# Optimization experiments

Hardware: AMD Instinct MI355X
Metric: run time of the kernel (lower is better)

## Reference

```python
import jax, jax.numpy as jnp
import numpy as np

EPS = 1e-5
P = 8  # patch size


def ln_chan(x, w, b):
    # LayerNorm over channel dim C of (B,C,H,W): per-pixel mean/var across channels
    mu = x.mean(axis=1, keepdims=True)
    var = x.var(axis=1, keepdims=True)
    return (x - mu) / jnp.sqrt(var + EPS) * w[None, :, None, None] + b[None, :, None, None]


def conv1x1(x, w):
    # w: (O, C) -> pointwise conv
    return jnp.einsum('bchw,oc->bohw', x, w)


def dwconv3(x, w):
    # depthwise 3x3, SAME padding; w: (C,1,3,3)
    return jax.lax.conv_general_dilated(
        x, w, window_strides=(1, 1), padding='SAME',
        dimension_numbers=('NCHW', 'OIHW', 'NCHW'),
        feature_group_count=x.shape[1])


def to_patches(t):
    b, c, h, w = t.shape
    return t.reshape(b, c, h // P, P, w // P, P).transpose(0, 1, 2, 4, 3, 5)


def from_patches(t, h, w):
    b, c = t.shape[:2]
    return t.transpose(0, 1, 2, 4, 3, 5).reshape(b, c, h, w)


def setup_inputs() -> dict:
    key = jax.random.key(0)
    ks = jax.random.split(key, 8)
    B, C, H, W = 4, 64, 256, 256
    s = 0.1  # weight scale to keep activations sane
    inp = {
        'x': jax.random.normal(ks[0], (B, C, H, W), jnp.float32),
        'evt': jax.random.normal(ks[1], (B, C, H, W), jnp.float32),
        'w_q': jax.random.normal(ks[2], (2 * C, C), jnp.float32) * s,
        'w_kv': jax.random.normal(ks[3], (4 * C, C), jnp.float32) * s,
        'w_qdw': jax.random.normal(ks[4], (2 * C, 1, 3, 3), jnp.float32) * s,
        'w_kvdw': jax.random.normal(ks[5], (4 * C, 1, 3, 3), jnp.float32) * s,
        'w_proj': jax.random.normal(ks[6], (C, 2 * C), jnp.float32) * s,
        'ln_img_w': jnp.ones((C,), jnp.float32),
        'ln_img_b': jnp.zeros((C,), jnp.float32),
        'ln_evt_w': jnp.ones((C,), jnp.float32),
        'ln_evt_b': jnp.zeros((C,), jnp.float32),
        'ln_out_w': jnp.ones((2 * C,), jnp.float32),
        'ln_out_b': jnp.zeros((2 * C,), jnp.float32),
    }
    return inp


def reference(x, evt, w_q, w_kv, w_qdw, w_kvdw, w_proj,
              ln_img_w, ln_img_b, ln_evt_w, ln_evt_b, ln_out_w, ln_out_b):
    x = ln_chan(x, ln_img_w, ln_img_b)
    evt = ln_chan(evt, ln_evt_w, ln_evt_b)
    q = dwconv3(conv1x1(x, w_q), w_qdw)          # (B, 2C, H, W)
    kv = dwconv3(conv1x1(evt, w_kv), w_kvdw)     # (B, 4C, H, W)
    k, v = jnp.split(kv, 2, axis=1)
    h, w = q.shape[-2:]
    q_fft = jnp.fft.rfft2(to_patches(q))         # (B,2C,h/8,w/8,8,5) complex
    k_fft = jnp.fft.rfft2(to_patches(k))
    out = jnp.fft.irfft2(q_fft * k_fft, s=(P, P))
    out = from_patches(out, h, w)                # (B, 2C, H, W)
    out = ln_chan(out, ln_out_w, ln_out_b)
    out = v * out
    return conv1x1(out, w_proj)                  # (B, C, H, W)
```

## Files before the change

### kernel.cpp

```cpp
#include <hip/hip_runtime.h>

typedef __attribute__((ext_vector_type(8))) short bf16x8;
typedef __attribute__((ext_vector_type(4))) float f32x4;
typedef __attribute__((ext_vector_type(2))) float f32x2;
typedef __attribute__((ext_vector_type(4))) unsigned int u32x4;
typedef __attribute__((ext_vector_type(2))) unsigned int u32x2;

__device__ __forceinline__ unsigned short f2bf(float f) {
    union { float f; unsigned int u; } v; v.f = f;
    return (unsigned short)((v.u + 0x7fffu + ((v.u >> 16) & 1u)) >> 16);
}
__device__ __forceinline__ float bflo(unsigned int u) {
    union { unsigned int u; float f; } v; v.u = u << 16; return v.f;
}
__device__ __forceinline__ float bfhi(unsigned int u) {
    union { unsigned int u; float f; } v; v.u = u & 0xffff0000u; return v.f;
}
__device__ __forceinline__ f32x2 bfpair(unsigned int u) {
    union { unsigned int u; float f; } lo, hi;
    lo.u = u << 16; hi.u = u & 0xffff0000u;
    return (f32x2){lo.f, hi.f};
}

__device__ __forceinline__ unsigned short costab(int m) {
    unsigned short mag = (m & 1) ? 0x3F35 : (((m & 3) == 0) ? 0x3F80 : 0);
    return mag | (((m >= 3) && (m <= 5)) ? 0x8000 : 0);
}
__device__ __forceinline__ unsigned short nsintab(int m) {
    unsigned short mag = (m & 1) ? 0x3F35 : (((m & 3) == 2) ? 0x3F80 : 0);
    return mag | (((m >= 1) && (m <= 3)) ? 0x8000 : 0);
}

__device__ __forceinline__ float wred_allsum(float x) {
    asm volatile(
        "s_nop 1\n\t"
        "v_add_f32_dpp %0, %0, %0 row_shr:1 bound_ctrl:0\n\t"
        "s_nop 1\n\t"
        "v_add_f32_dpp %0, %0, %0 row_shr:2 bound_ctrl:0\n\t"
        "s_nop 1\n\t"
        "v_add_f32_dpp %0, %0, %0 row_shr:4 bound_ctrl:0\n\t"
        "s_nop 1\n\t"
        "v_add_f32_dpp %0, %0, %0 row_shr:8 bound_ctrl:0\n\t"
        "s_nop 1\n\t"
        "v_add_f32_dpp %0, %0, %0 row_bcast:15 row_mask:0xa bound_ctrl:0\n\t"
        "s_nop 1\n\t"
        "v_add_f32_dpp %0, %0, %0 row_bcast:31 row_mask:0xc bound_ctrl:0\n\t"
        "s_nop 1"
        : "+v"(x));
    return __builtin_bit_cast(float, __builtin_amdgcn_readlane(__builtin_bit_cast(int, x), 63));
}

__global__ __launch_bounds__(256, 8)
void ln_kernel(const float* __restrict__ x, const float* __restrict__ evt,
               const float* __restrict__ lwx, const float* __restrict__ lbx,
               const float* __restrict__ lwe, const float* __restrict__ lbe,
               unsigned short* __restrict__ xo, unsigned short* __restrict__ eo)
{
    __shared__ float xt[64][68];
    __shared__ float ps[4][64], ps2[4][64];
    __shared__ float smu[64], sinv[64], slw[64], slb[64];

    const int tid = threadIdx.x;
    const int z = blockIdx.z, b = blockIdx.y;
    const int hw0 = blockIdx.x * 64;
    const float* src = z ? evt : x;
    const float* lw  = z ? lwe : lwx;
    const float* lb  = z ? lbe : lbx;
    unsigned short* dst = z ? eo : xo;

    if (tid < 64) { slw[tid] = lw[tid]; slb[tid] = lb[tid]; }

    const float* sp = src + (size_t)b * 64 * 65536 + hw0;
    #pragma unroll
    for (int it = 0; it < 4; ++it) {
        int i = tid + it * 256;
        int c = i >> 4, p4 = i & 15;
        f32x4 v = *(const f32x4*)&sp[(size_t)c * 65536 + p4 * 4];
        xt[p4 * 4 + 0][c] = v.x;
        xt[p4 * 4 + 1][c] = v.y;
        xt[p4 * 4 + 2][c] = v.z;
        xt[p4 * 4 + 3][c] = v.w;
    }
    __syncthreads();

    {
        int px = tid & 63, part = tid >> 6;
        float s = 0.f, s2 = 0.f;
        #pragma unroll
        for (int j = 0; j < 4; ++j) {
            f32x4 v = *(const f32x4*)&xt[px][part * 16 + j * 4];
            s  += v.x + v.y + v.z + v.w;
            s2 += v.x * v.x + v.y * v.y + v.z * v.z + v.w * v.w;
        }
        ps[part][px] = s; ps2[part][px] = s2;
    }
    __syncthreads();
    if (tid < 64) {
        float s  = ps[0][tid] + ps[1][tid] + ps[2][tid] + ps[3][tid];
        float s2 = ps2[0][tid] + ps2[1][tid] + ps2[2][tid] + ps2[3][tid];
        float mu = s * (1.f / 64.f);
        smu[tid] = mu;
        sinv[tid] = rsqrtf(s2 * (1.f / 64.f) - mu * mu + 1e-5f);
    }
    __syncthreads();

    unsigned short* dp = dst + ((size_t)b * 65536 + hw0) * 64;
    #pragma unroll
    for (int it = 0; it < 2; ++it) {
        int i = tid + it * 256;
        int px = i >> 3, oct = i & 7;
        float mu = smu[px], inv = sinv[px];
        f32x4 v0 = *(const f32x4*)&xt[px][oct * 8];
        f32x4 v1 = *(const f32x4*)&xt[px][oct * 8 + 4];
        u32x4 w;
        int c = oct * 8;
        float a0 = (v0.x - mu) * inv * slw[c + 0] + slb[c + 0];
        float a1 = (v0.y - mu) * inv * slw[c + 1] + slb[c + 1];
        w[0] = (unsigned int)f2bf(a0) | ((unsigned int)f2bf(a1) << 16);
        a0 = (v0.z - mu) * inv * slw[c + 2] + slb[c + 2];
        a1 = (v0.w - mu) * inv * slw[c + 3] + slb[c + 3];
        w[1] = (unsigned int)f2bf(a0) | ((unsigned int)f2bf(a1) << 16);
        a0 = (v1.x - mu) * inv * slw[c + 4] + slb[c + 4];
        a1 = (v1.y - mu) * inv * slw[c + 5] + slb[c + 5];
        w[2] = (unsigned int)f2bf(a0) | ((unsigned int)f2bf(a1) << 16);
        a0 = (v1.z - mu) * inv * slw[c + 6] + slb[c + 6];
        a1 = (v1.w - mu) * inv * slw[c + 7] + slb[c + 7];
        w[3] = (unsigned int)f2bf(a0) | ((unsigned int)f2bf(a1) << 16);
        *(u32x4*)&dp[(size_t)px * 64 + oct * 8] = w;
    }
}

#define PR_WB    14336
#define PR_WDW   30720
#define PR_SMEM  35328

__global__ __launch_bounds__(512, 8)
void prod_kernel(const unsigned short* __restrict__ src,
                 const float* __restrict__ wmat, const float* __restrict__ wdw,
                 unsigned short* __restrict__ dst)
{
    __shared__ __align__(16) char smem[PR_SMEM];
    unsigned short* A   = (unsigned short*)(smem);
    unsigned short* Wb  = (unsigned short*)(smem + PR_WB);
    unsigned short* pre = (unsigned short*)(smem);
    float* swdw = (float*)(smem + PR_WDW);

    const int tid = threadIdx.x;
    const int pj = blockIdx.x, pi = blockIdx.y, b = blockIdx.z;
    const int h0 = pi * 8, w0 = pj * 8;

    #pragma unroll
    for (int it = 0; it < 4; ++it) {
        int i = tid + it * 512;
        int o = i >> 4, c4 = i & 15;
        f32x4 wv = *(const f32x4*)&wmat[o * 64 + c4 * 4];
        unsigned int lo = (unsigned int)f2bf(wv[0]) | ((unsigned int)f2bf(wv[1]) << 16);
        unsigned int hi = (unsigned int)f2bf(wv[2]) | ((unsigned int)f2bf(wv[3]) << 16);
        u32x2 pk = {lo, hi};
        *(u32x2*)&Wb[o * 64 + (((c4 >> 1) ^ (o & 7)) << 3) + (c4 & 1) * 4] = pk;
    }
    for (int i = tid; i < 1152; i += 512) swdw[i] = wdw[i];
    for (int i = tid; i < 768; i += 512) A[6400 + i] = 0;
    #pragma unroll
    for (int it = 0; it < 2; ++it) {
        int i = tid + it * 512;
        if (i < 800) {
            int px = i >> 3, oct = i & 7;
            int r = px / 10, cc = px - r * 10;
            int gh = h0 - 1 + r, gw = w0 - 1 + cc;
            u32x4 val = {0u, 0u, 0u, 0u};
            if (gh >= 0 && gh < 256 && gw >= 0 && gw < 256)
                val = *(const u32x4*)&src[((size_t)(b * 65536 + gh * 256 + gw)) * 64 + oct * 8];
            *(u32x4*)&A[px * 64 + ((oct ^ (px & 7)) << 3)] = val;
        }
    }
    __syncthreads();

    const int lane = tid & 63;
    const int l15 = lane & 15, l4 = lane >> 4;
    const int o_n = (tid >> 6) * 16 + l15;
    f32x4 acc[7];
    #pragma unroll
    for (int mt = 0; mt < 7; ++mt) acc[mt] = (f32x4){0.f, 0.f, 0.f, 0.f};
    #pragma unroll
    for (int ks = 0; ks < 2; ++ks) {
        int cch = ks * 4 + l4;
        bf16x8 bfrag = *(const bf16x8*)&Wb[o_n * 64 + ((cch ^ (o_n & 7)) << 3)];
        #pragma unroll
        for (int mt = 0; mt < 7; ++mt) {
            int px = mt * 16 + l15;
            bf16x8 afrag = *(const bf16x8*)&A[px * 64 + ((cch ^ (px & 7)) << 3)];
            acc[mt] = __builtin_amdgcn_mfma_f32_16x16x32_bf16(afrag, bfrag, acc[mt], 0, 0, 0);
        }
    }
    __syncthreads();

    #pragma unroll
    for (int mt = 0; mt < 7; ++mt)
        #pragma unroll
        for (int r = 0; r < 4; ++r) {
            int px = mt * 16 + l4 * 4 + r;
            if (px < 100)
                pre[px * 128 + (((o_n >> 3) ^ (px & 7)) << 3) + (o_n & 7)] = f2bf(acc[mt][r]);
        }
    __syncthreads();

    f32x2 res[8];
    {
        const int o = (tid & 63) * 2;
        const int och = o >> 3, osub = o & 7;
        const int pc = tid >> 6;
        f32x2 wdp[9];
        #pragma unroll
        for (int t = 0; t < 9; ++t)
            wdp[t] = (f32x2){swdw[o * 9 + t], swdw[o * 9 + 9 + t]};

        f32x2 ra[3], rb[3], rc[3];
        #define LOADROW(dstv, rr)                                                        \
            {                                                                            \
                _Pragma("unroll")                                                        \
                for (int d = 0; d < 3; ++d) {                                            \
                    int hp = (rr) * 10 + pc + d;                                         \
                    unsigned int u = *(const unsigned int*)                              \
                        &pre[hp * 128 + ((och ^ (hp & 7)) << 3) + osub];                 \
                    dstv[d] = bfpair(u);                                                 \
                }                                                                        \
            }
        LOADROW(ra, 0)
        LOADROW(rb, 1)
        #pragma unroll
        for (int r = 2; r < 10; ++r) {
            LOADROW(rc, r)
            f32x2 s = ra[0] * wdp[0];
            s += ra[1] * wdp[1]; s += ra[2] * wdp[2];
            s += rb[0] * wdp[3]; s += rb[1] * wdp[4]; s += rb[2] * wdp[5];
            s += rc[0] * wdp[6]; s += rc[1] * wdp[7]; s += rc[2] * wdp[8];
            res[r - 2] = s;
            #pragma unroll
            for (int d = 0; d < 3; ++d) { ra[d] = rb[d]; rb[d] = rc[d]; }
        }
        #undef LOADROW
    }
    __syncthreads();

    {
        unsigned short* ldout = (unsigned short*)smem;
        const int o = (tid & 63) * 2;
        const int pc = tid >> 6;
        const int key = pc << 4;
        #pragma unroll
        for (int r = 0; r < 8; ++r) {
            int px = r * 8 + pc;
            unsigned int pk = (unsigned int)f2bf(res[r].x) | ((unsigned int)f2bf(res[r].y) << 16);
            *(unsigned int*)&ldout[px * 128 + (o ^ key)] = pk;
        }
    }
    __syncthreads();

    {
        unsigned short* ldout = (unsigned short*)smem;
        const int c0 = (tid & 63) * 2;
        const int s = tid >> 6;
        const int sl0 = s ^ (c0 & 7);
        const int sl1 = s ^ ((c0 + 1) & 7);
        const size_t patchbase = ((size_t)(b * 32 + pi) * 32 + pj) * 8192;
        unsigned int rv[8];
        #pragma unroll
        for (int j = 0; j < 8; ++j)
            rv[j] = *(const unsigned int*)&ldout[(8 * s + j) * 128 + (c0 ^ (j << 4))];
        u32x4 lo, hi;
        #pragma unroll
        for (int d = 0; d < 4; ++d) {
            lo[d] = (rv[2 * d] & 0xffffu) | (rv[2 * d + 1] << 16);
            hi[d] = (rv[2 * d] >> 16) | (rv[2 * d + 1] & 0xffff0000u);
        }
        *(u32x4*)&dst[patchbase + (size_t)c0 * 64 + sl0 * 8]       = lo;
        *(u32x4*)&dst[patchbase + (size_t)(c0 + 1) * 64 + sl1 * 8] = hi;
    }
}

#define PK_R0   0
#define PK_R1   16384
#define PK_F    32768
#define PK_WP   49152
#define PK_LW   65536
#define PK_LB   66048
#define PK_SMEM 66560

__global__ __launch_bounds__(512, 4)
void patch_kernel(const unsigned short* __restrict__ qb,
                  const unsigned short* __restrict__ kb,
                  const unsigned short* __restrict__ vb,
                  const float* __restrict__ w_proj,
                  const float* __restrict__ lnw, const float* __restrict__ lnb,
                  float* __restrict__ out)
{
    __shared__ __align__(16) char smem[PK_SMEM];
    unsigned short* sqT  = (unsigned short*)(smem + PK_R0);
    unsigned short* skT  = (unsigned short*)(smem + PK_R1);
    unsigned short* ohr  = sqT;
    unsigned short* ohi  = skT;
    float*          out2 = (float*)smem;
    unsigned short* sFre = (unsigned short*)(smem + PK_F);
    unsigned short* sFim = (unsigned short*)(smem + PK_F + 8192);
    unsigned short* swp  = (unsigned short*)(smem + PK_WP);
    unsigned short* sy   = (unsigned short*)(smem + PK_R1);
    float*          sc   = (float*)(smem + PK_R0);
    float* slw = (float*)(smem + PK_LW);
    float* slb = (float*)(smem + PK_LB);

    const int tid = threadIdx.x;
    const int tj = blockIdx.x, ti = blockIdx.y, b = blockIdx.z;
    const int h0 = ti * 8, w0 = tj * 8;
    const size_t pbase = ((size_t)(b * 32 + ti) * 32 + tj) * 8192;

    const int pr = tid >> 6;
    const int cq = tid & 63;

    u32x4 vreg0 = *(const u32x4*)&vb[pbase + (2 * cq) * 64 + ((pr ^ ((2 * cq) & 7)) << 3)];
    u32x4 vreg1 = *(const u32x4*)&vb[pbase + (2 * cq + 1) * 64 + ((pr ^ ((2 * cq + 1) & 7)) << 3)];

    if (tid < 128) { slw[tid] = lnw[tid]; slb[tid] = lnb[tid]; }
    #pragma unroll
    for (int it = 0; it < 2; ++it) {
        int i = tid + it * 512;
        *(u32x4*)&sqT[i * 8] = *(const u32x4*)&qb[pbase + i * 8];
        *(u32x4*)&skT[i * 8] = *(const u32x4*)&kb[pbase + i * 8];
    }
    #pragma unroll
    for (int it = 0; it < 4; ++it) {
        int i = tid + it * 512;
        int o = i >> 5, c4 = i & 31;
        f32x4 wv = *(const f32x4*)&w_proj[o * 128 + c4 * 4];
        unsigned int lo = (unsigned int)f2bf(wv[0]) | ((unsigned int)f2bf(wv[1]) << 16);
        unsigned int hi = (unsigned int)f2bf(wv[2]) | ((unsigned int)f2bf(wv[3]) << 16);
        u32x2 pk = {lo, hi};
        *(u32x2*)&swp[o * 128 + (((c4 >> 1) ^ (o & 7)) << 3) + (c4 & 1) * 4] = pk;
    }
    #pragma unroll
    for (int it = 0; it < 8; ++it) {
        int i = tid + it * 512;
        int f = i >> 6, t = i & 63;
        int m = ((f >> 3) * (t >> 3) + (f & 7) * (t & 7)) & 7;
        int pos = f * 64 + ((((t >> 3) ^ (f & 7)) << 3)) + (t & 7);
        sFre[pos] = costab(m);
        sFim[pos] = nsintab(m);
    }
    __syncthreads();

    const int lane = tid & 63;
    const int l15 = lane & 15, l4 = lane >> 4;
    const int wid = tid >> 6;
    const int ntile = wid >> 1;
    const int mtbase = (wid & 1) * 4;
    const int fcol = ntile * 16 + l15;

    bf16x8 bre[2], bim[2];
    #pragma unroll
    for (int ks = 0; ks < 2; ++ks) {
        int cch = ks * 4 + l4;
        int off = fcol * 64 + ((cch ^ (fcol & 7)) << 3);
        bre[ks] = *(const bf16x8*)&sFre[off];
        bim[ks] = *(const bf16x8*)&sFim[off];
    }
    f32x4 fr_[4], fi_[4];
    #pragma unroll
    for (int mt = 0; mt < 4; ++mt) {
        const int crow = (mtbase + mt) * 16 + l15;
        bf16x8 aq[2], ak[2];
        #pragma unroll
        for (int ks = 0; ks < 2; ++ks) {
            int cch = ks * 4 + l4;
            int off = crow * 64 + ((cch ^ (crow & 7)) << 3);
            aq[ks] = *(const bf16x8*)&sqT[off];
            ak[ks] = *(const bf16x8*)&skT[off];
        }
        f32x4 qr = {0.f,0.f,0.f,0.f}, qi = qr, kr = qr, ki = qr;
        qr = __builtin_amdgcn_mfma_f32_16x16x32_bf16(aq[0], bre[0], qr, 0, 0, 0);
        qr = __builtin_amdgcn_mfma_f32_16x16x32_bf16(aq[1], bre[1], qr, 0, 0, 0);
        qi = __builtin_amdgcn_mfma_f32_16x16x32_bf16(aq[0], bim[0], qi, 0, 0, 0);
        qi = __builtin_amdgcn_mfma_f32_16x16x32_bf16(aq[1], bim[1], qi, 0, 0, 0);
        kr = __builtin_amdgcn_mfma_f32_16x16x32_bf16(ak[0], bre[0], kr, 0, 0, 0);
        kr = __builtin_amdgcn_mfma_f32_16x16x32_bf16(ak[1], bre[1], kr, 0, 0, 0);
        ki = __builtin_amdgcn_mfma_f32_16x16x32_bf16(ak[0], bim[0], ki, 0, 0, 0);
        ki = __builtin_amdgcn_mfma_f32_16x16x32_bf16(ak[1], bim[1], ki, 0, 0, 0);
        fr_[mt] = (qr * kr - qi * ki) * 0.015625f;
        fi_[mt] = (qr * ki + qi * kr) * 0.015625f;
    }
    __syncthreads();

    #pragma unroll
    for (int mt = 0; mt < 4; ++mt)
        #pragma unroll
        for (int r = 0; r < 4; ++r) {
            int c = (mtbase + mt) * 16 + l4 * 4 + r;
            int pos = c * 64 + (((fcol >> 3) ^ (c & 7)) << 3) + (fcol & 7);
            ohr[pos] = f2bf(fr_[mt][r]);
            ohi[pos] = f2bf(fi_[mt][r]);
        }
    __syncthreads();

    const int prow = ntile * 16 + l15;
    bf16x8 gre[2], gim[2];
    #pragma unroll
    for (int ks = 0; ks < 2; ++ks) {
        int cch = ks * 4 + l4;
        int off = prow * 64 + ((cch ^ (prow & 7)) << 3);
        gre[ks] = *(const bf16x8*)&sFre[off];
        gim[ks] = *(const bf16x8*)&sFim[off];
    }
    f32x4 oreg[4];
    #pragma unroll
    for (int mt = 0; mt < 4; ++mt) {
        const int crow = (mtbase + mt) * 16 + l15;
        bf16x8 ar[2], ai[2];
        #pragma unroll
        for (int ks = 0; ks < 2; ++ks) {
            int cch = ks * 4 + l4;
            int off = crow * 64 + ((cch ^ (crow & 7)) << 3);
            ar[ks] = *(const bf16x8*)&ohr[off];
            ai[ks] = *(const bf16x8*)&ohi[off];
        }
        f32x4 o2 = {0.f,0.f,0.f,0.f};
        o2 = __builtin_amdgcn_mfma_f32_16x16x32_bf16(ar[0], gre[0], o2, 0, 0, 0);
        o2 = __builtin_amdgcn_mfma_f32_16x16x32_bf16(ar[1], gre[1], o2, 0, 0, 0);
        o2 = __builtin_amdgcn_mfma_f32_16x16x32_bf16(ai[0], gim[0], o2, 0, 0, 0);
        o2 = __builtin_amdgcn_mfma_f32_16x16x32_bf16(ai[1], gim[1], o2, 0, 0, 0);
        oreg[mt] = o2;
    }
    __syncthreads();

    #pragma unroll
    for (int mt = 0; mt < 4; ++mt) {
        int c0 = (mtbase + mt) * 16 + l4 * 4;
        *(f32x4*)&out2[prow * 128 + (c0 ^ ((prow & 7) << 2))] = oreg[mt];
    }
    __syncthreads();

    const float lw0 = slw[2 * cq], lw1 = slw[2 * cq + 1];
    const float lb0 = slb[2 * cq], lb1 = slb[2 * cq + 1];
    f32x2 acc[8];
    #pragma unroll
    for (int pc = 0; pc < 8; ++pc) {
        int px = pr * 8 + pc;
        acc[pc] = *(const f32x2*)&out2[px * 128 + ((2 * cq) ^ ((px & 7) << 2))];
    }
    float mu[8], inv[8];
    #pragma unroll
    for (int pc = 0; pc < 8; ++pc) {
        float s  = wred_allsum(acc[pc].x + acc[pc].y);
        float s2 = wred_allsum(acc[pc].x * acc[pc].x + acc[pc].y * acc[pc].y);
        float m_ = s * (1.f / 128.f);
        mu[pc]  = m_;
        inv[pc] = rsqrtf(s2 * (1.f / 128.f) - m_ * m_ + 1e-5f);
    }
    __syncthreads();

    #pragma unroll
    for (int pc = 0; pc < 8; ++pc) {
        int px = pr * 8 + pc;
        const int d = pc >> 1;
        f32x2 vp = (pc & 1) ? (f32x2){bfhi(vreg0[d]), bfhi(vreg1[d])}
                            : (f32x2){bflo(vreg0[d]), bflo(vreg1[d])};
        float y0 = ((acc[pc].x - mu[pc]) * inv[pc] * lw0 + lb0) * vp.x;
        float y1 = ((acc[pc].y - mu[pc]) * inv[pc] * lw1 + lb1) * vp.y;
        unsigned int pk = (unsigned int)f2bf(y0) | ((unsigned int)f2bf(y1) << 16);
        *(unsigned int*)&sy[px * 128 + (((cq >> 2) ^ (px & 7)) << 3) + 2 * (cq & 3)] = pk;
    }
    __syncthreads();

    {
        const int mt = wid >> 1;
        const int nt0 = 2 * (wid & 1);
        f32x4 pacc[2];
        pacc[0] = (f32x4){0.f, 0.f, 0.f, 0.f};
        pacc[1] = (f32x4){0.f, 0.f, 0.f, 0.f};
        const int px_a = mt * 16 + l15;
        #pragma unroll
        for (int ks = 0; ks < 4; ++ks) {
            int cch = ks * 4 + l4;
            bf16x8 af = *(const bf16x8*)&sy[px_a * 128 + ((cch ^ (px_a & 7)) << 3)];
            #pragma unroll
            for (int p2 = 0; p2 < 2; ++p2) {
                int o_n = (nt0 + p2) * 16 + l15;
                bf16x8 bfr = *(const bf16x8*)&swp[o_n * 128 + ((cch ^ (o_n & 7)) << 3)];
                pacc[p2] = __builtin_amdgcn_mfma_f32_16x16x32_bf16(af, bfr, pacc[p2], 0, 0, 0);
            }
        }
        #pragma unroll
        for (int p2 = 0; p2 < 2; ++p2)
            #pragma unroll
            for (int r = 0; r < 4; ++r) {
                int px = mt * 16 + l4 * 4 + r;
                int o = (nt0 + p2) * 16 + l15;
                sc[px * 64 + o] = pacc[p2][r];
            }
    }
    __syncthreads();

    {
        const int o = tid & 63, r = tid >> 6;
        float v0[4], v1[4];
        #pragma unroll
        for (int j = 0; j < 4; ++j) {
            v0[j] = sc[(r * 8 + j) * 64 + o];
            v1[j] = sc[(r * 8 + 4 + j) * 64 + o];
        }
        int obase = ((b * 64 + o) * 256 + h0 + r) * 256 + w0;
        *(f32x4*)&out[obase]     = (f32x4){v0[0], v0[1], v0[2], v0[3]};
        *(f32x4*)&out[obase + 4] = (f32x4){v1[0], v1[1], v1[2], v1[3]};
    }
}

extern "C" void kernel_launch(void* const* d_in, const int* in_sizes, int n_in,
                              void* d_out, int out_size, void* d_ws, size_t ws_size,
                              hipStream_t stream) {
    (void)in_sizes; (void)n_in; (void)out_size; (void)ws_size;
    const float* x        = (const float*)d_in[0];
    const float* evt      = (const float*)d_in[1];
    const float* w_q      = (const float*)d_in[2];
    const float* w_kv     = (const float*)d_in[3];
    const float* w_qdw    = (const float*)d_in[4];
    const float* w_kvdw   = (const float*)d_in[5];
    const float* w_proj   = (const float*)d_in[6];
    const float* ln_img_w = (const float*)d_in[7];
    const float* ln_img_b = (const float*)d_in[8];
    const float* ln_evt_w = (const float*)d_in[9];
    const float* ln_evt_b = (const float*)d_in[10];
    const float* ln_out_w = (const float*)d_in[11];
    const float* ln_out_b = (const float*)d_in[12];
    float* out = (float*)d_out;

    const size_t NPATCH = (size_t)4 * 32 * 32 * 8192;
    const size_t NLN    = (size_t)4 * 65536 * 64;
    unsigned short* qd  = (unsigned short*)d_ws;
    unsigned short* kd  = qd + NPATCH;
    unsigned short* eln = kd + NPATCH;
    unsigned short* xln = eln + NLN;
    unsigned short* vd  = xln;

    dim3 lgrid(1024, 4, 2), lblk(256);
    ln_kernel<<<lgrid, lblk, 0, stream>>>(x, evt, ln_img_w, ln_img_b,
                                          ln_evt_w, ln_evt_b, xln, eln);
    dim3 grid(32, 32, 4), blk(512);
    prod_kernel<<<grid, blk, 0, stream>>>(xln, w_q,            w_qdw,           qd);
    prod_kernel<<<grid, blk, 0, stream>>>(eln, w_kv,           w_kvdw,          kd);
    prod_kernel<<<grid, blk, 0, stream>>>(eln, w_kv + 128*64,  w_kvdw + 128*9,  vd);
    patch_kernel<<<grid, blk, 0, stream>>>(qd, kd, vd, w_proj, ln_out_w, ln_out_b, out);
}
```

Measured before the change: 282.7 us.

## Compute DFT twiddle fragments in registers and drop the shared-memory tables

New measurement: 331.5 us. 1.17x slower.

```diff
diff --git a/kernel.cpp b/kernel.cpp
--- a/kernel.cpp
+++ b/kernel.cpp
@@ -29,6 +29,20 @@
 __device__ __forceinline__ unsigned short nsintab(int m) {
     unsigned short mag = (m & 1) ? 0x3F35 : (((m & 3) == 2) ? 0x3F80 : 0);
     return mag | (((m >= 1) && (m <= 3)) ? 0x8000 : 0);
+}
+__device__ __forceinline__ bf16x8 ffrag(int fcol, int cch, bool im) {
+    const int base = ((fcol >> 3) * cch) & 7;
+    const int step = fcol & 7;
+    union { unsigned int u[4]; bf16x8 v; } cv;
+    #pragma unroll
+    for (int d = 0; d < 4; ++d) {
+        int m0 = (base + step * (2 * d)) & 7;
+        int m1 = (base + step * (2 * d + 1)) & 7;
+        unsigned short t0 = im ? nsintab(m0) : costab(m0);
+        unsigned short t1 = im ? nsintab(m1) : costab(m1);
+        cv.u[d] = (unsigned int)t0 | ((unsigned int)t1 << 16);
+    }
+    return cv.v;
 }
 
 __device__ __forceinline__ float wred_allsum(float x) {
@@ -57,7 +71,6 @@
                unsigned short* __restrict__ xo, unsigned short* __restrict__ eo)
 {
     __shared__ float xt[64][68];
-    __shared__ float ps[4][64], ps2[4][64];
     __shared__ float smu[64], sinv[64], slw[64], slb[64];
 
     const int tid = threadIdx.x;
@@ -84,7 +97,7 @@
     __syncthreads();
 
     {
-        int px = tid & 63, part = tid >> 6;
+        int px = tid >> 2, part = tid & 3;
         float s = 0.f, s2 = 0.f;
         #pragma unroll
         for (int j = 0; j < 4; ++j) {
@@ -92,15 +105,13 @@
             s  += v.x + v.y + v.z + v.w;
             s2 += v.x * v.x + v.y * v.y + v.z * v.z + v.w * v.w;
         }
-        ps[part][px] = s; ps2[part][px] = s2;
-    }
-    __syncthreads();
-    if (tid < 64) {
-        float s  = ps[0][tid] + ps[1][tid] + ps[2][tid] + ps[3][tid];
-        float s2 = ps2[0][tid] + ps2[1][tid] + ps2[2][tid] + ps2[3][tid];
-        float mu = s * (1.f / 64.f);
-        smu[tid] = mu;
-        sinv[tid] = rsqrtf(s2 * (1.f / 64.f) - mu * mu + 1e-5f);
+        s  += __shfl_xor(s, 1);  s  += __shfl_xor(s, 2);
+        s2 += __shfl_xor(s2, 1); s2 += __shfl_xor(s2, 2);
+        if (part == 0) {
+            float mu = s * (1.f / 64.f);
+            smu[px] = mu;
+            sinv[px] = rsqrtf(s2 * (1.f / 64.f) - mu * mu + 1e-5f);
+        }
     }
     __syncthreads();
 
@@ -281,13 +292,12 @@
 
 #define PK_R0   0
 #define PK_R1   16384
-#define PK_F    32768
-#define PK_WP   49152
-#define PK_LW   65536
-#define PK_LB   66048
-#define PK_SMEM 66560
-
-__global__ __launch_bounds__(512, 4)
+#define PK_WP   32768
+#define PK_LW   49152
+#define PK_LB   49664
+#define PK_SMEM 50176
+
+__global__ __launch_bounds__(512, 6)
 void patch_kernel(const unsigned short* __restrict__ qb,
                   const unsigned short* __restrict__ kb,
                   const unsigned short* __restrict__ vb,
@@ -301,8 +311,6 @@
     unsigned short* ohr  = sqT;
     unsigned short* ohi  = skT;
     float*          out2 = (float*)smem;
-    unsigned short* sFre = (unsigned short*)(smem + PK_F);
-    unsigned short* sFim = (unsigned short*)(smem + PK_F + 8192);
     unsigned short* swp  = (unsigned short*)(smem + PK_WP);
     unsigned short* sy   = (unsigned short*)(smem + PK_R1);
     float*          sc   = (float*)(smem + PK_R0);
@@ -337,16 +345,6 @@
         u32x2 pk = {lo, hi};
         *(u32x2*)&swp[o * 128 + (((c4 >> 1) ^ (o & 7)) << 3) + (c4 & 1) * 4] = pk;
     }
-    #pragma unroll
-    for (int it = 0; it < 8; ++it) {
-        int i = tid + it * 512;
-        int f = i >> 6, t = i & 63;
-        int m = ((f >> 3) * (t >> 3) + (f & 7) * (t & 7)) & 7;
-        int pos = f * 64 + ((((t >> 3) ^ (f & 7)) << 3)) + (t & 7);
-        sFre[pos] = costab(m);
-        sFim[pos] = nsintab(m);
-    }
-    __syncthreads();
 
     const int lane = tid & 63;
     const int l15 = lane & 15, l4 = lane >> 4;
@@ -359,10 +357,11 @@
     #pragma unroll
     for (int ks = 0; ks < 2; ++ks) {
         int cch = ks * 4 + l4;
-        int off = fcol * 64 + ((cch ^ (fcol & 7)) << 3);
-        bre[ks] = *(const bf16x8*)&sFre[off];
-        bim[ks] = *(const bf16x8*)&sFim[off];
-    }
+        bre[ks] = ffrag(fcol, cch, false);
+        bim[ks] = ffrag(fcol, cch, true);
+    }
+    __syncthreads();
+
     f32x4 fr_[4], fi_[4];
     #pragma unroll
     for (int mt = 0; mt < 4; ++mt) {
@@ -400,15 +399,6 @@
         }
     __syncthreads();
 
-    const int prow = ntile * 16 + l15;
-    bf16x8 gre[2], gim[2];
-    #pragma unroll
-    for (int ks = 0; ks < 2; ++ks) {
-        int cch = ks * 4 + l4;
-        int off = prow * 64 + ((cch ^ (prow & 7)) << 3);
-        gre[ks] = *(const bf16x8*)&sFre[off];
-        gim[ks] = *(const bf16x8*)&sFim[off];
-    }
     f32x4 oreg[4];
     #pragma unroll
     for (int mt = 0; mt < 4; ++mt) {
@@ -422,14 +412,15 @@
             ai[ks] = *(const bf16x8*)&ohi[off];
         }
         f32x4 o2 = {0.f,0.f,0.f,0.f};
-        o2 = __builtin_amdgcn_mfma_f32_16x16x32_bf16(ar[0], gre[0], o2, 0, 0, 0);
-        o2 = __builtin_amdgcn_mfma_f32_16x16x32_bf16(ar[1], gre[1], o2, 0, 0, 0);
-        o2 = __builtin_amdgcn_mfma_f32_16x16x32_bf16(ai[0], gim[0], o2, 0, 0, 0);
-        o2 = __builtin_amdgcn_mfma_f32_16x16x32_bf16(ai[1], gim[1], o2, 0, 0, 0);
+        o2 = __builtin_amdgcn_mfma_f32_16x16x32_bf16(ar[0], bre[0], o2, 0, 0, 0);
+        o2 = __builtin_amdgcn_mfma_f32_16x16x32_bf16(ar[1], bre[1], o2, 0, 0, 0);
+        o2 = __builtin_amdgcn_mfma_f32_16x16x32_bf16(ai[0], bim[0], o2, 0, 0, 0);
+        o2 = __builtin_amdgcn_mfma_f32_16x16x32_bf16(ai[1], bim[1], o2, 0, 0, 0);
         oreg[mt] = o2;
     }
     __syncthreads();
 
+    const int prow = fcol;
     #pragma unroll
     for (int mt = 0; mt < 4; ++mt) {
         int c0 = (mtbase + mt) * 16 + l4 * 4;
```
